# Kernel tuning notes

Hardware: AMD Instinct MI355X
Metric: run time of the kernel (lower is better)

The kernel has to match this reference:

```python
import jax, jax.numpy as jnp
import numpy as np


def _resize_bilinear_align_corners(x, out_size):
    # x: [B, C, h, w] -> [B, C, out_size, out_size], matches F.interpolate(mode='bilinear', align_corners=True)
    def axis_interp(arr, size_in, size_out, axis):
        coords = jnp.linspace(0.0, size_in - 1.0, size_out)
        i0 = jnp.floor(coords).astype(jnp.int32)
        i1 = jnp.minimum(i0 + 1, size_in - 1)
        t = (coords - i0).astype(arr.dtype)
        a0 = jnp.take(arr, i0, axis=axis)
        a1 = jnp.take(arr, i1, axis=axis)
        shape = [1] * arr.ndim
        shape[axis] = size_out
        t = t.reshape(shape)
        return a0 * (1.0 - t) + a1 * t

    B, C, h, w = x.shape
    x = axis_interp(x, h, out_size, 2)
    x = axis_interp(x, w, out_size, 3)
    return x


def _similarity_matrix(x, sp, num):
    # Torch: mean_values[i][j] = mean(x[i][sp_repeated[i] == j], dim=0)
    # Boolean indexing flattens across channels, so this is a SCALAR mean over
    # (channels x segment pixels), broadcast to all C channels.
    B, C, H, W = x.shape
    xs = x.sum(axis=1).reshape(B, H * W)          # sum over channels, per pixel
    ids = sp.reshape(B, H * W)
    seg_sum = jax.vmap(
        lambda v, i: jax.ops.segment_sum(v, i, num_segments=num))(xs, ids)
    cnt = jax.vmap(
        lambda i: jax.ops.segment_sum(jnp.ones(i.shape, x.dtype), i,
                                      num_segments=num))(ids)
    m = seg_sum / (cnt * C)                        # [B, num] scalar mean per segment
    # diff vector over channels has identical entries -> norm(diff)/sqrt(C) == |m_i - m_j|
    return 1.0 - jnp.abs(m[:, :, None] - m[:, None, :])  # [B, num, num]


def reference(input, feature, sp, num):
    feature = _resize_bilinear_align_corners(feature, input.shape[-1])
    mat1 = _similarity_matrix(input, sp, num)
    mat2 = _similarity_matrix(feature, sp, num)
    return jnp.mean(jnp.abs(mat1 - mat2))


def setup_inputs() -> dict:
    key = jax.random.key(0)
    k1, k2, k3 = jax.random.split(key, 3)
    B, C_in, H, W = 8, 64, 256, 256
    C_feat, hf, wf = 256, 64, 64
    num = 256
    return {
        "input": jax.random.normal(k1, (B, C_in, H, W), dtype=jnp.float32),
        "feature": jax.random.normal(k2, (B, C_feat, hf, wf), dtype=jnp.float32),
        "sp": jax.random.randint(k3, (B, 1, H, W), 0, num, dtype=jnp.int32),
        "num": num,
    }
```

## Files before the change

### kernel.cpp

```cpp
#include <hip/hip_runtime.h>

#define NB 8
#define C_IN 64
#define HW 65536
#define CF 256
#define FHW 4096
#define NSEG 256
#define NGRP 8
#define MBLK 64


__global__ void featsum_kernel(const float* __restrict__ feat,
                               float* __restrict__ partial) {
    int b = blockIdx.y, g = blockIdx.z;
    int q = blockIdx.x * 256 + threadIdx.x;
    const float4* f4 = (const float4*)(feat + ((size_t)(b * CF + g * 32)) * FHW);
    float4 s = make_float4(0.f, 0.f, 0.f, 0.f);
#pragma unroll
    for (int c = 0; c < 32; ++c) {
        float4 v = f4[(size_t)c * (FHW / 4) + q];
        s.x += v.x; s.y += v.y; s.z += v.z; s.w += v.w;
    }
    ((float4*)partial)[(size_t)(b * NGRP + g) * (FHW / 4) + q] = s;
}

__global__ __launch_bounds__(256) void main_kernel(
    const float* __restrict__ input, const int* __restrict__ sp,
    const float* __restrict__ partial, float* __restrict__ seg_part) {
    __shared__ float fls[FHW];
    __shared__ float bin[3][NSEG];
    int b = blockIdx.y;
    int t = threadIdx.x;
    const float4* p4 = (const float4*)(partial + (size_t)b * NGRP * FHW);
    for (int i = t; i < FHW / 4; i += 256) {
        float4 s = p4[i];
#pragma unroll
        for (int g = 1; g < NGRP; ++g) {
            float4 v = p4[g * (FHW / 4) + i];
            s.x += v.x; s.y += v.y; s.z += v.z; s.w += v.w;
        }
        ((float4*)fls)[i] = s;
    }
    bin[0][t] = 0.f; bin[1][t] = 0.f; bin[2][t] = 0.f;
    __syncthreads();

    int p0 = blockIdx.x * 1024 + t * 4;
    int v0 = blockIdx.x * 256 + t;
    const float4* in4 = (const float4*)(input + (size_t)b * C_IN * HW);
    float4 xs = make_float4(0.f, 0.f, 0.f, 0.f);
#pragma unroll
    for (int c = 0; c < C_IN; ++c) {
        float4 v = in4[(size_t)c * (HW / 4) + v0];
        xs.x += v.x; xs.y += v.y; xs.z += v.z; xs.w += v.w;
    }
    int4 sv = ((const int4*)(sp + (size_t)b * HW))[v0];

    int y = p0 >> 8;
    float cy = (float)y * (63.0f / 255.0f);
    int iy = (int)cy; float ty = cy - (float)iy; int iy1 = min(iy + 1, 63);
    float xsv[4] = {xs.x, xs.y, xs.z, xs.w};
    int   ssv[4] = {sv.x, sv.y, sv.z, sv.w};
#pragma unroll
    for (int k = 0; k < 4; ++k) {
        int x = (p0 + k) & 255;
        float cx = (float)x * (63.0f / 255.0f);
        int ix = (int)cx; float tx = cx - (float)ix; int ix1 = min(ix + 1, 63);
        float f00 = fls[iy * 64 + ix],  f10 = fls[iy1 * 64 + ix];
        float f01 = fls[iy * 64 + ix1], f11 = fls[iy1 * 64 + ix1];
        float a0 = f00 * (1.f - ty) + f10 * ty;
        float a1 = f01 * (1.f - ty) + f11 * ty;
        float fs = a0 * (1.f - tx) + a1 * tx;
        int s = ssv[k];
        atomicAdd(&bin[0][s], xsv[k]);
        atomicAdd(&bin[1][s], fs);
        atomicAdd(&bin[2][s], 1.f);
    }
    __syncthreads();
    float* sb = seg_part + (size_t)(b * MBLK + blockIdx.x) * 3 * NSEG;
    sb[t]            = bin[0][t];
    sb[NSEG + t]     = bin[1][t];
    sb[2 * NSEG + t] = bin[2][t];
}

__global__ __launch_bounds__(1024) void pair_kernel(
    const float* __restrict__ seg_part, float* __restrict__ pp) {
    __shared__ float s3[3 * NSEG];
    __shared__ float m1[NSEG], m2[NSEG];
    __shared__ float red[16];
    int b = blockIdx.x, t = threadIdx.x;
    if (t < 3 * NSEG) {
        float s = 0.f;
        const float* base = seg_part + (size_t)b * MBLK * 3 * NSEG + t;
#pragma unroll 8
        for (int k = 0; k < MBLK; ++k) s += base[(size_t)k * 3 * NSEG];
        s3[t] = s;
    }
    __syncthreads();
    if (t < NSEG) {
        float cnt = s3[2 * NSEG + t];
        m1[t] = s3[t] / (cnt * 64.0f);
        m2[t] = s3[NSEG + t] / (cnt * 256.0f);
    }
    __syncthreads();
    int i = t & 255;
    int j0 = (t >> 8) * 64;
    float a1 = m1[i], a2 = m2[i];
    float acc = 0.f;
#pragma unroll 8
    for (int jj = 0; jj < 64; ++jj) {
        int j = j0 + jj;
        acc += fabsf(fabsf(a1 - m1[j]) - fabsf(a2 - m2[j]));
    }
#pragma unroll
    for (int off = 32; off; off >>= 1) acc += __shfl_down(acc, off);
    if ((t & 63) == 0) red[t >> 6] = acc;
    __syncthreads();
    if (t == 0) {
        float s = 0.f;
#pragma unroll
        for (int w = 0; w < 16; ++w) s += red[w];
        pp[b] = s;
    }
}

__global__ void final_kernel(const float* __restrict__ pp,
                             float* __restrict__ out) {
    int t = threadIdx.x;
    float v = (t < NB) ? pp[t] : 0.f;
#pragma unroll
    for (int off = 4; off; off >>= 1) v += __shfl_down(v, off);
    if (t == 0) out[0] = v / 524288.0f;
}

extern "C" void kernel_launch(void* const* d_in, const int* in_sizes, int n_in,
                              void* d_out, int out_size, void* d_ws, size_t ws_size,
                              hipStream_t stream) {
    const float* input   = (const float*)d_in[0];
    const float* feature = (const float*)d_in[1];
    const int*   sp      = (const int*)d_in[2];
    float* ws = (float*)d_ws;
    float* partial  = ws;
    float* seg_part = ws + (size_t)NB * NGRP * FHW;
    float* pp       = seg_part + (size_t)NB * MBLK * 3 * NSEG;

    featsum_kernel<<<dim3(4, 8, 8), 256, 0, stream>>>(feature, partial);
    main_kernel<<<dim3(MBLK, 8), 256, 0, stream>>>(input, sp, partial, seg_part);
    pair_kernel<<<dim3(8), 1024, 0, stream>>>(seg_part, pp);
    final_kernel<<<1, 64, 0, stream>>>(pp, (float*)d_out);
}
```

Measured before the change: 49.79 us.

## Fuse four launches into two kernels with a spin-flag final reduction

```diff
diff --git a/kernel.cpp b/kernel.cpp
--- a/kernel.cpp
+++ b/kernel.cpp
@@ -8,143 +8,165 @@
 #define NSEG 256
 #define NGRP 8
 #define MBLK 64
+#define MAGIC 0x13579BDFu
 
 
-__global__ void featsum_kernel(const float* __restrict__ feat,
-                               float* __restrict__ partial) {
-    int b = blockIdx.y, g = blockIdx.z;
-    int q = blockIdx.x * 256 + threadIdx.x;
+__global__ __launch_bounds__(256) void k1(
+    const float* __restrict__ input, const int* __restrict__ sp,
+    const float* __restrict__ feat,
+    float* __restrict__ partial, float* __restrict__ seg_part) {
+  int b = blockIdx.y, t = threadIdx.x;
+  if (blockIdx.x >= MBLK) {
+    int e = blockIdx.x - MBLK;
+    int g = e >> 1, half = e & 1;
     const float4* f4 = (const float4*)(feat + ((size_t)(b * CF + g * 32)) * FHW);
-    float4 s = make_float4(0.f, 0.f, 0.f, 0.f);
+    float4* o4 = (float4*)partial + (size_t)(b * NGRP + g) * (FHW / 4);
 #pragma unroll
-    for (int c = 0; c < 32; ++c) {
+    for (int j = 0; j < 2; ++j) {
+      int q = half * 512 + j * 256 + t;
+      float4 s = make_float4(0.f, 0.f, 0.f, 0.f);
+#pragma unroll
+      for (int c = 0; c < 32; ++c) {
         float4 v = f4[(size_t)c * (FHW / 4) + q];
         s.x += v.x; s.y += v.y; s.z += v.z; s.w += v.w;
+      }
+      o4[q] = s;
     }
-    ((float4*)partial)[(size_t)(b * NGRP + g) * (FHW / 4) + q] = s;
+    return;
+  }
+  __shared__ float bin_x[NSEG], bin_c[NSEG];
+  bin_x[t] = 0.f; bin_c[t] = 0.f;
+  __syncthreads();
+  int v0 = blockIdx.x * 256 + t;
+  const float4* in4 = (const float4*)(input + (size_t)b * C_IN * HW);
+  float4 xs = make_float4(0.f, 0.f, 0.f, 0.f);
+#pragma unroll
+  for (int c = 0; c < C_IN; ++c) {
+    float4 v = in4[(size_t)c * (HW / 4) + v0];
+    xs.x += v.x; xs.y += v.y; xs.z += v.z; xs.w += v.w;
+  }
+  int4 sv = ((const int4*)(sp + (size_t)b * HW))[v0];
+  atomicAdd(&bin_x[sv.x], xs.x); atomicAdd(&bin_c[sv.x], 1.f);
+  atomicAdd(&bin_x[sv.y], xs.y); atomicAdd(&bin_c[sv.y], 1.f);
+  atomicAdd(&bin_x[sv.z], xs.z); atomicAdd(&bin_c[sv.z], 1.f);
+  atomicAdd(&bin_x[sv.w], xs.w); atomicAdd(&bin_c[sv.w], 1.f);
+  __syncthreads();
+  float* sb = seg_part + (size_t)(b * MBLK + blockIdx.x) * 2 * NSEG;
+  sb[t] = bin_x[t];
+  sb[NSEG + t] = bin_c[t];
 }
 
-__global__ __launch_bounds__(256) void main_kernel(
-    const float* __restrict__ input, const int* __restrict__ sp,
-    const float* __restrict__ partial, float* __restrict__ seg_part) {
-    __shared__ float fls[FHW];
-    __shared__ float bin[3][NSEG];
-    int b = blockIdx.y;
-    int t = threadIdx.x;
+__global__ __launch_bounds__(1024) void k2(
+    const int* __restrict__ sp, const float* __restrict__ partial,
+    const float* __restrict__ seg_part,
+    unsigned* __restrict__ ppbits, unsigned* __restrict__ flags,
+    float* __restrict__ out) {
+  __shared__ float fls[FHW];
+  __shared__ float segs[2 * NSEG];
+  __shared__ float binf[NSEG];
+  __shared__ float m1[NSEG], m2[NSEG];
+  __shared__ float red[16];
+  int b = blockIdx.x, t = threadIdx.x;
+
+  {
     const float4* p4 = (const float4*)(partial + (size_t)b * NGRP * FHW);
-    for (int i = t; i < FHW / 4; i += 256) {
-        float4 s = p4[i];
+    float4 s = p4[t];
 #pragma unroll
-        for (int g = 1; g < NGRP; ++g) {
-            float4 v = p4[g * (FHW / 4) + i];
-            s.x += v.x; s.y += v.y; s.z += v.z; s.w += v.w;
-        }
-        ((float4*)fls)[i] = s;
+    for (int g = 1; g < NGRP; ++g) {
+      float4 v = p4[g * (FHW / 4) + t];
+      s.x += v.x; s.y += v.y; s.z += v.z; s.w += v.w;
     }
-    bin[0][t] = 0.f; bin[1][t] = 0.f; bin[2][t] = 0.f;
-    __syncthreads();
+    ((float4*)fls)[t] = s;
+  }
+  if (t < 2 * NSEG) {
+    const float* base = seg_part + (size_t)b * MBLK * 2 * NSEG + t;
+    float s = 0.f;
+#pragma unroll 8
+    for (int k = 0; k < MBLK; ++k) s += base[(size_t)k * 2 * NSEG];
+    segs[t] = s;
+  }
+  if (t < NSEG) binf[t] = 0.f;
+  __syncthreads();
 
-    int p0 = blockIdx.x * 1024 + t * 4;
-    int v0 = blockIdx.x * 256 + t;
-    const float4* in4 = (const float4*)(input + (size_t)b * C_IN * HW);
-    float4 xs = make_float4(0.f, 0.f, 0.f, 0.f);
-#pragma unroll
-    for (int c = 0; c < C_IN; ++c) {
-        float4 v = in4[(size_t)c * (HW / 4) + v0];
-        xs.x += v.x; xs.y += v.y; xs.z += v.z; xs.w += v.w;
-    }
-    int4 sv = ((const int4*)(sp + (size_t)b * HW))[v0];
-
+  const int4* sp4 = (const int4*)(sp + (size_t)b * HW);
+#pragma unroll 4
+  for (int k = 0; k < 16; ++k) {
+    int v4 = k * 1024 + t;
+    int4 sv = sp4[v4];
+    int p0 = v4 * 4;
     int y = p0 >> 8;
     float cy = (float)y * (63.0f / 255.0f);
     int iy = (int)cy; float ty = cy - (float)iy; int iy1 = min(iy + 1, 63);
-    float xsv[4] = {xs.x, xs.y, xs.z, xs.w};
-    int   ssv[4] = {sv.x, sv.y, sv.z, sv.w};
+    int svv[4] = {sv.x, sv.y, sv.z, sv.w};
 #pragma unroll
-    for (int k = 0; k < 4; ++k) {
-        int x = (p0 + k) & 255;
-        float cx = (float)x * (63.0f / 255.0f);
-        int ix = (int)cx; float tx = cx - (float)ix; int ix1 = min(ix + 1, 63);
-        float f00 = fls[iy * 64 + ix],  f10 = fls[iy1 * 64 + ix];
-        float f01 = fls[iy * 64 + ix1], f11 = fls[iy1 * 64 + ix1];
-        float a0 = f00 * (1.f - ty) + f10 * ty;
-        float a1 = f01 * (1.f - ty) + f11 * ty;
-        float fs = a0 * (1.f - tx) + a1 * tx;
-        int s = ssv[k];
-        atomicAdd(&bin[0][s], xsv[k]);
-        atomicAdd(&bin[1][s], fs);
-        atomicAdd(&bin[2][s], 1.f);
+    for (int kk = 0; kk < 4; ++kk) {
+      int x = (p0 + kk) & 255;
+      float cx = (float)x * (63.0f / 255.0f);
+      int ix = (int)cx; float tx = cx - (float)ix; int ix1 = min(ix + 1, 63);
+      float f00 = fls[iy * 64 + ix],  f10 = fls[iy1 * 64 + ix];
+      float f01 = fls[iy * 64 + ix1], f11 = fls[iy1 * 64 + ix1];
+      float a0 = f00 * (1.f - ty) + f10 * ty;
+      float a1 = f01 * (1.f - ty) + f11 * ty;
+      atomicAdd(&binf[svv[kk]], a0 * (1.f - tx) + a1 * tx);
     }
-    __syncthreads();
-    float* sb = seg_part + (size_t)(b * MBLK + blockIdx.x) * 3 * NSEG;
-    sb[t]            = bin[0][t];
-    sb[NSEG + t]     = bin[1][t];
-    sb[2 * NSEG + t] = bin[2][t];
-}
+  }
+  __syncthreads();
+  if (t < NSEG) {
+    float cnt = segs[NSEG + t];
+    m1[t] = segs[t] / (cnt * 64.0f);
+    m2[t] = binf[t] / (cnt * 256.0f);
+  }
+  __syncthreads();
 
-__global__ __launch_bounds__(1024) void pair_kernel(
-    const float* __restrict__ seg_part, float* __restrict__ pp) {
-    __shared__ float s3[3 * NSEG];
-    __shared__ float m1[NSEG], m2[NSEG];
-    __shared__ float red[16];
-    int b = blockIdx.x, t = threadIdx.x;
-    if (t < 3 * NSEG) {
-        float s = 0.f;
-        const float* base = seg_part + (size_t)b * MBLK * 3 * NSEG + t;
+  int i = t & 255, j0 = (t >> 8) * 64;
+  float a1 = m1[i], a2 = m2[i], acc = 0.f;
 #pragma unroll 8
-        for (int k = 0; k < MBLK; ++k) s += base[(size_t)k * 3 * NSEG];
-        s3[t] = s;
+  for (int jj = 0; jj < 64; ++jj) {
+    int j = j0 + jj;
+    acc += fabsf(fabsf(a1 - m1[j]) - fabsf(a2 - m2[j]));
+  }
+#pragma unroll
+  for (int off = 32; off; off >>= 1) acc += __shfl_down(acc, off);
+  if ((t & 63) == 0) red[t >> 6] = acc;
+  __syncthreads();
+
+  if (t == 0) {
+    float s = 0.f;
+#pragma unroll
+    for (int w = 0; w < 16; ++w) s += red[w];
+    __hip_atomic_store(&ppbits[b], __float_as_uint(s), __ATOMIC_RELAXED,
+                       __HIP_MEMORY_SCOPE_AGENT);
+    __hip_atomic_store(&flags[b], MAGIC, __ATOMIC_RELEASE,
+                       __HIP_MEMORY_SCOPE_AGENT);
+    if (b == 0) {
+      float tot = s;
+      for (int ob = 1; ob < NB; ++ob) {
+        while (__hip_atomic_load(&flags[ob], __ATOMIC_ACQUIRE,
+                                 __HIP_MEMORY_SCOPE_AGENT) != MAGIC) {}
+        tot += __uint_as_float(__hip_atomic_load(
+            &ppbits[ob], __ATOMIC_RELAXED, __HIP_MEMORY_SCOPE_AGENT));
+      }
+      out[0] = tot / 524288.0f;
+      for (int ob = 0; ob < NB; ++ob)
+        __hip_atomic_store(&flags[ob], 0u, __ATOMIC_RELAXED,
+                           __HIP_MEMORY_SCOPE_AGENT);
     }
-    __syncthreads();
-    if (t < NSEG) {
-        float cnt = s3[2 * NSEG + t];
-        m1[t] = s3[t] / (cnt * 64.0f);
-        m2[t] = s3[NSEG + t] / (cnt * 256.0f);
-    }
-    __syncthreads();
-    int i = t & 255;
-    int j0 = (t >> 8) * 64;
-    float a1 = m1[i], a2 = m2[i];
-    float acc = 0.f;
-#pragma unroll 8
-    for (int jj = 0; jj < 64; ++jj) {
-        int j = j0 + jj;
-        acc += fabsf(fabsf(a1 - m1[j]) - fabsf(a2 - m2[j]));
-    }
-#pragma unroll
-    for (int off = 32; off; off >>= 1) acc += __shfl_down(acc, off);
-    if ((t & 63) == 0) red[t >> 6] = acc;
-    __syncthreads();
-    if (t == 0) {
-        float s = 0.f;
-#pragma unroll
-        for (int w = 0; w < 16; ++w) s += red[w];
-        pp[b] = s;
-    }
-}
-
-__global__ void final_kernel(const float* __restrict__ pp,
-                             float* __restrict__ out) {
-    int t = threadIdx.x;
-    float v = (t < NB) ? pp[t] : 0.f;
-#pragma unroll
-    for (int off = 4; off; off >>= 1) v += __shfl_down(v, off);
-    if (t == 0) out[0] = v / 524288.0f;
+  }
 }
 
 extern "C" void kernel_launch(void* const* d_in, const int* in_sizes, int n_in,
                               void* d_out, int out_size, void* d_ws, size_t ws_size,
                               hipStream_t stream) {
-    const float* input   = (const float*)d_in[0];
-    const float* feature = (const float*)d_in[1];
-    const int*   sp      = (const int*)d_in[2];
-    float* ws = (float*)d_ws;
-    float* partial  = ws;
-    float* seg_part = ws + (size_t)NB * NGRP * FHW;
-    float* pp       = seg_part + (size_t)NB * MBLK * 3 * NSEG;
+  const float* input   = (const float*)d_in[0];
+  const float* feature = (const float*)d_in[1];
+  const int*   sp      = (const int*)d_in[2];
+  float* ws = (float*)d_ws;
+  float*    partial  = ws;
+  float*    seg_part = ws + (size_t)NB * NGRP * FHW;
+  unsigned* ppbits   = (unsigned*)(seg_part + (size_t)NB * MBLK * 2 * NSEG);
+  unsigned* flags    = ppbits + NB;
 
-    featsum_kernel<<<dim3(4, 8, 8), 256, 0, stream>>>(feature, partial);
-    main_kernel<<<dim3(MBLK, 8), 256, 0, stream>>>(input, sp, partial, seg_part);
-    pair_kernel<<<dim3(8), 1024, 0, stream>>>(seg_part, pp);
-    final_kernel<<<1, 64, 0, stream>>>(pp, (float*)d_out);
+  k1<<<dim3(MBLK + 16, NB), 256, 0, stream>>>(input, sp, feature, partial, seg_part);
+  k2<<<dim3(NB), 1024, 0, stream>>>(sp, partial, seg_part, ppbits, flags,
+                                    (float*)d_out);
 }
```

New measurement: 129.8 us. 161% more time.

## Fully reduce feature channels in featsum and fuse final reduction into pair kernel

Applied to the files above, without the earlier changes.

```diff
diff --git a/kernel.cpp b/kernel.cpp
--- a/kernel.cpp
+++ b/kernel.cpp
@@ -6,145 +6,154 @@
 #define CF 256
 #define FHW 4096
 #define NSEG 256
-#define NGRP 8
 #define MBLK 64
+#define MAGIC 0x13579BDFu
+#define AG __HIP_MEMORY_SCOPE_AGENT
 
 
-__global__ void featsum_kernel(const float* __restrict__ feat,
-                               float* __restrict__ partial) {
-    int b = blockIdx.y, g = blockIdx.z;
-    int q = blockIdx.x * 256 + threadIdx.x;
-    const float4* f4 = (const float4*)(feat + ((size_t)(b * CF + g * 32)) * FHW);
-    float4 s = make_float4(0.f, 0.f, 0.f, 0.f);
-#pragma unroll
-    for (int c = 0; c < 32; ++c) {
-        float4 v = f4[(size_t)c * (FHW / 4) + q];
-        s.x += v.x; s.y += v.y; s.z += v.z; s.w += v.w;
-    }
-    ((float4*)partial)[(size_t)(b * NGRP + g) * (FHW / 4) + q] = s;
+__global__ __launch_bounds__(256) void featsum_kernel(
+    const float* __restrict__ feat, float* __restrict__ fsum) {
+  __shared__ float4 lred[256];
+  int b = blockIdx.y, e = blockIdx.x, t = threadIdx.x;
+  int q = t & 63, cg = t >> 6;
+  const float4* f4 = (const float4*)(feat + (size_t)b * CF * FHW);
+  int col = e * 64 + q;
+  float4 s = make_float4(0.f, 0.f, 0.f, 0.f);
+#pragma unroll 8
+  for (int c = cg; c < CF; c += 4) {
+    float4 v = f4[(size_t)c * (FHW / 4) + col];
+    s.x += v.x; s.y += v.y; s.z += v.z; s.w += v.w;
+  }
+  lred[cg * 64 + q] = s;
+  __syncthreads();
+  if (t < 64) {
+    float4 a = lred[t], b1 = lred[64 + t], c1 = lred[128 + t], d = lred[192 + t];
+    a.x += b1.x + c1.x + d.x; a.y += b1.y + c1.y + d.y;
+    a.z += b1.z + c1.z + d.z; a.w += b1.w + c1.w + d.w;
+    ((float4*)fsum)[(size_t)b * (FHW / 4) + e * 64 + t] = a;
+  }
 }
 
 __global__ __launch_bounds__(256) void main_kernel(
     const float* __restrict__ input, const int* __restrict__ sp,
-    const float* __restrict__ partial, float* __restrict__ seg_part) {
-    __shared__ float fls[FHW];
-    __shared__ float bin[3][NSEG];
-    int b = blockIdx.y;
-    int t = threadIdx.x;
-    const float4* p4 = (const float4*)(partial + (size_t)b * NGRP * FHW);
-    for (int i = t; i < FHW / 4; i += 256) {
-        float4 s = p4[i];
+    const float* __restrict__ fsum, float* __restrict__ seg_part) {
+  __shared__ float fls[FHW];
+  __shared__ float bin[3][NSEG];
+  int b = blockIdx.y, blk = blockIdx.x, t = threadIdx.x;
+  {
+    const float4* s4 = (const float4*)(fsum + (size_t)b * FHW);
+    float4* d4 = (float4*)fls;
 #pragma unroll
-        for (int g = 1; g < NGRP; ++g) {
-            float4 v = p4[g * (FHW / 4) + i];
-            s.x += v.x; s.y += v.y; s.z += v.z; s.w += v.w;
-        }
-        ((float4*)fls)[i] = s;
-    }
-    bin[0][t] = 0.f; bin[1][t] = 0.f; bin[2][t] = 0.f;
-    __syncthreads();
+    for (int i = 0; i < 4; ++i) d4[i * 256 + t] = s4[i * 256 + t];
+  }
+  bin[0][t] = 0.f; bin[1][t] = 0.f; bin[2][t] = 0.f;
+  __syncthreads();
 
-    int p0 = blockIdx.x * 1024 + t * 4;
-    int v0 = blockIdx.x * 256 + t;
-    const float4* in4 = (const float4*)(input + (size_t)b * C_IN * HW);
-    float4 xs = make_float4(0.f, 0.f, 0.f, 0.f);
+  int v0 = blk * 256 + t;
+  const float4* in4 = (const float4*)(input + (size_t)b * C_IN * HW);
+  float4 xs = make_float4(0.f, 0.f, 0.f, 0.f);
 #pragma unroll
-    for (int c = 0; c < C_IN; ++c) {
-        float4 v = in4[(size_t)c * (HW / 4) + v0];
-        xs.x += v.x; xs.y += v.y; xs.z += v.z; xs.w += v.w;
-    }
-    int4 sv = ((const int4*)(sp + (size_t)b * HW))[v0];
+  for (int c = 0; c < C_IN; ++c) {
+    float4 v = in4[(size_t)c * (HW / 4) + v0];
+    xs.x += v.x; xs.y += v.y; xs.z += v.z; xs.w += v.w;
+  }
+  int4 sv = ((const int4*)(sp + (size_t)b * HW))[v0];
+  atomicAdd(&bin[0][sv.x], xs.x); atomicAdd(&bin[1][sv.x], 1.f);
+  atomicAdd(&bin[0][sv.y], xs.y); atomicAdd(&bin[1][sv.y], 1.f);
+  atomicAdd(&bin[0][sv.z], xs.z); atomicAdd(&bin[1][sv.z], 1.f);
+  atomicAdd(&bin[0][sv.w], xs.w); atomicAdd(&bin[1][sv.w], 1.f);
 
-    int y = p0 >> 8;
-    float cy = (float)y * (63.0f / 255.0f);
-    int iy = (int)cy; float ty = cy - (float)iy; int iy1 = min(iy + 1, 63);
-    float xsv[4] = {xs.x, xs.y, xs.z, xs.w};
-    int   ssv[4] = {sv.x, sv.y, sv.z, sv.w};
+  int p0 = v0 * 4;
+  int y = p0 >> 8;
+  float cy = (float)y * (63.0f / 255.0f);
+  int iy = (int)cy; float ty = cy - (float)iy; int iy1 = min(iy + 1, 63);
+  int svv[4] = {sv.x, sv.y, sv.z, sv.w};
 #pragma unroll
-    for (int k = 0; k < 4; ++k) {
-        int x = (p0 + k) & 255;
-        float cx = (float)x * (63.0f / 255.0f);
-        int ix = (int)cx; float tx = cx - (float)ix; int ix1 = min(ix + 1, 63);
-        float f00 = fls[iy * 64 + ix],  f10 = fls[iy1 * 64 + ix];
-        float f01 = fls[iy * 64 + ix1], f11 = fls[iy1 * 64 + ix1];
-        float a0 = f00 * (1.f - ty) + f10 * ty;
-        float a1 = f01 * (1.f - ty) + f11 * ty;
-        float fs = a0 * (1.f - tx) + a1 * tx;
-        int s = ssv[k];
-        atomicAdd(&bin[0][s], xsv[k]);
-        atomicAdd(&bin[1][s], fs);
-        atomicAdd(&bin[2][s], 1.f);
-    }
-    __syncthreads();
-    float* sb = seg_part + (size_t)(b * MBLK + blockIdx.x) * 3 * NSEG;
-    sb[t]            = bin[0][t];
-    sb[NSEG + t]     = bin[1][t];
-    sb[2 * NSEG + t] = bin[2][t];
+  for (int kk = 0; kk < 4; ++kk) {
+    int x = (p0 + kk) & 255;
+    float cx = (float)x * (63.0f / 255.0f);
+    int ix = (int)cx; float tx = cx - (float)ix; int ix1 = min(ix + 1, 63);
+    float f00 = fls[iy * 64 + ix],  f10 = fls[iy1 * 64 + ix];
+    float f01 = fls[iy * 64 + ix1], f11 = fls[iy1 * 64 + ix1];
+    float a0 = f00 * (1.f - ty) + f10 * ty;
+    float a1 = f01 * (1.f - ty) + f11 * ty;
+    atomicAdd(&bin[2][svv[kk]], a0 * (1.f - tx) + a1 * tx);
+  }
+  __syncthreads();
+  float* sb = seg_part + (size_t)(b * MBLK + blk) * 3 * NSEG;
+  sb[t]            = bin[0][t];
+  sb[NSEG + t]     = bin[1][t];
+  sb[2 * NSEG + t] = bin[2][t];
 }
 
-__global__ __launch_bounds__(1024) void pair_kernel(
-    const float* __restrict__ seg_part, float* __restrict__ pp) {
-    __shared__ float s3[3 * NSEG];
-    __shared__ float m1[NSEG], m2[NSEG];
-    __shared__ float red[16];
-    int b = blockIdx.x, t = threadIdx.x;
-    if (t < 3 * NSEG) {
-        float s = 0.f;
-        const float* base = seg_part + (size_t)b * MBLK * 3 * NSEG + t;
-#pragma unroll 8
-        for (int k = 0; k < MBLK; ++k) s += base[(size_t)k * 3 * NSEG];
-        s3[t] = s;
+__global__ __launch_bounds__(1024) void pairfinal_kernel(
+    const float* __restrict__ seg_part,
+    unsigned* __restrict__ ppbits, unsigned* __restrict__ bflags,
+    float* __restrict__ out) {
+  __shared__ float s3[3 * NSEG];
+  __shared__ float m1[NSEG], m2[NSEG];
+  __shared__ float red[16];
+  int b = blockIdx.x, t = threadIdx.x;
+  if (t < 3 * NSEG) {
+    const float* base = seg_part + (size_t)b * MBLK * 3 * NSEG + t;
+    float s = 0.f;
+#pragma unroll
+    for (int k = 0; k < MBLK; ++k) s += base[k * 3 * NSEG];
+    s3[t] = s;
+  }
+  __syncthreads();
+  if (t < NSEG) {
+    float cnt = s3[NSEG + t];
+    m1[t] = s3[t] / (cnt * 64.0f);
+    m2[t] = s3[2 * NSEG + t] / (cnt * 256.0f);
+  }
+  __syncthreads();
+  int i = t & 255, j0 = (t >> 8) * 64;
+  float a1 = m1[i], a2 = m2[i], acc = 0.f;
+#pragma unroll
+  for (int jj = 0; jj < 64; ++jj) {
+    int j = j0 + jj;
+    acc += fabsf(fabsf(a1 - m1[j]) - fabsf(a2 - m2[j]));
+  }
+#pragma unroll
+  for (int off = 32; off; off >>= 1) acc += __shfl_down(acc, off);
+  if ((t & 63) == 0) red[t >> 6] = acc;
+  __syncthreads();
+  if (t == 0) {
+    float s = 0.f;
+#pragma unroll
+    for (int w = 0; w < 16; ++w) s += red[w];
+    __hip_atomic_store(&ppbits[b], __float_as_uint(s), __ATOMIC_RELAXED, AG);
+    __hip_atomic_store(&bflags[b], MAGIC, __ATOMIC_RELEASE, AG);
+    if (b == 0) {
+      float tot = s;
+      for (int ob = 1; ob < NB; ++ob) {
+        while (__hip_atomic_load(&bflags[ob], __ATOMIC_ACQUIRE, AG) != MAGIC)
+          __builtin_amdgcn_s_sleep(2);
+        tot += __uint_as_float(__hip_atomic_load(
+            &ppbits[ob], __ATOMIC_RELAXED, AG));
+        __hip_atomic_store(&bflags[ob], 0u, __ATOMIC_RELAXED, AG);
+      }
+      out[0] = tot / 524288.0f;
+      __hip_atomic_store(&bflags[0], 0u, __ATOMIC_RELAXED, AG);
     }
-    __syncthreads();
-    if (t < NSEG) {
-        float cnt = s3[2 * NSEG + t];
-        m1[t] = s3[t] / (cnt * 64.0f);
-        m2[t] = s3[NSEG + t] / (cnt * 256.0f);
-    }
-    __syncthreads();
-    int i = t & 255;
-    int j0 = (t >> 8) * 64;
-    float a1 = m1[i], a2 = m2[i];
-    float acc = 0.f;
-#pragma unroll 8
-    for (int jj = 0; jj < 64; ++jj) {
-        int j = j0 + jj;
-        acc += fabsf(fabsf(a1 - m1[j]) - fabsf(a2 - m2[j]));
-    }
-#pragma unroll
-    for (int off = 32; off; off >>= 1) acc += __shfl_down(acc, off);
-    if ((t & 63) == 0) red[t >> 6] = acc;
-    __syncthreads();
-    if (t == 0) {
-        float s = 0.f;
-#pragma unroll
-        for (int w = 0; w < 16; ++w) s += red[w];
-        pp[b] = s;
-    }
-}
-
-__global__ void final_kernel(const float* __restrict__ pp,
-                             float* __restrict__ out) {
-    int t = threadIdx.x;
-    float v = (t < NB) ? pp[t] : 0.f;
-#pragma unroll
-    for (int off = 4; off; off >>= 1) v += __shfl_down(v, off);
-    if (t == 0) out[0] = v / 524288.0f;
+  }
 }
 
 extern "C" void kernel_launch(void* const* d_in, const int* in_sizes, int n_in,
                               void* d_out, int out_size, void* d_ws, size_t ws_size,
                               hipStream_t stream) {
-    const float* input   = (const float*)d_in[0];
-    const float* feature = (const float*)d_in[1];
-    const int*   sp      = (const int*)d_in[2];
-    float* ws = (float*)d_ws;
-    float* partial  = ws;
-    float* seg_part = ws + (size_t)NB * NGRP * FHW;
-    float* pp       = seg_part + (size_t)NB * MBLK * 3 * NSEG;
+  const float* input   = (const float*)d_in[0];
+  const float* feature = (const float*)d_in[1];
+  const int*   sp      = (const int*)d_in[2];
+  float* ws = (float*)d_ws;
+  float*    fsum     = ws;
+  float*    seg_part = ws + (size_t)NB * FHW;
+  unsigned* ppbits   = (unsigned*)(seg_part + (size_t)NB * MBLK * 3 * NSEG);
+  unsigned* bflags   = ppbits + NB;
 
-    featsum_kernel<<<dim3(4, 8, 8), 256, 0, stream>>>(feature, partial);
-    main_kernel<<<dim3(MBLK, 8), 256, 0, stream>>>(input, sp, partial, seg_part);
-    pair_kernel<<<dim3(8), 1024, 0, stream>>>(seg_part, pp);
-    final_kernel<<<1, 64, 0, stream>>>(pp, (float*)d_out);
+  featsum_kernel<<<dim3(16, NB), 256, 0, stream>>>(feature, fsum);
+  main_kernel<<<dim3(MBLK, NB), 256, 0, stream>>>(input, sp, fsum, seg_part);
+  pairfinal_kernel<<<dim3(NB), 1024, 0, stream>>>(seg_part, ppbits, bflags,
+                                                  (float*)d_out);
 }
```

Measured after the change: 50.54 us. Within noise of the previous version (+1.5%).
